# Optimization experiments

Hardware: AMD Instinct MI355X
Metric: run time of the kernel (lower is better)

## Reference

```python
import jax, jax.numpy as jnp
import numpy as np

B, S, D = 2, 2048, 1024
E, N, HID = 8, 4, 4096

def setup_inputs() -> dict:
    key = jax.random.key(0)
    ks = jax.random.split(key, 6)
    x = jax.random.normal(ks[0], (B, S, D), dtype=jnp.float32)
    w_router = jax.random.normal(ks[1], (E, D), dtype=jnp.float32) * 0.02
    A_fc = jax.random.normal(ks[2], (E, N, N, N), dtype=jnp.float32) * 0.5
    S_fc = jax.random.normal(ks[3], (E, N, HID // N, D // N), dtype=jnp.float32) * (1.0 / np.sqrt(D))
    A_proj = jax.random.normal(ks[4], (E, N, N, N), dtype=jnp.float32) * 0.5
    S_proj = jax.random.normal(ks[5], (E, N, D // N, HID // N), dtype=jnp.float32) * (1.0 / np.sqrt(HID))
    return {"x": x, "w_router": w_router, "A_fc": A_fc, "S_fc": S_fc, "A_proj": A_proj, "S_proj": S_proj}

def _phm(Xn, A, S):
    # Xn: [T, n, s_in], S: [n, s_out, s_in], A: [n, n, n] -> [T, n, s_out]
    T_ = jnp.einsum('bkl,iol->bkio', Xn, S)
    return jnp.einsum('ijk,bkio->bjo', A, T_)

def reference(x, w_router, A_fc, S_fc, A_proj, S_proj):
    e_num, n = A_fc.shape[0], A_fc.shape[1]
    d = x.shape[-1]
    flat = x.reshape(-1, d)                      # [T, D]
    T = flat.shape[0]
    logits = flat @ w_router.T                   # [T, E]
    probs = jax.nn.softmax(logits, axis=-1)
    expert_idx = jnp.argmax(logits, axis=-1)     # [T]
    tpe = jnp.zeros((e_num,), flat.dtype).at[expert_idx].add(1.0)
    frac = tpe / T
    aux_loss = jnp.sum(frac * probs.mean(axis=0)) * e_num
    Xn = flat.reshape(T, n, d // n)
    out = jnp.zeros_like(flat)
    for e in range(e_num):                        # small fixed expert loop
        h = _phm(Xn, A_fc[e], S_fc[e]).reshape(T, -1)   # [T, HID]
        h = jnp.where(h >= 0, h, 0.5 * h)               # leaky_relu slope 0.5
        Hn = (h * h).reshape(T, n, -1)
        y = _phm(Hn, A_proj[e], S_proj[e]).reshape(T, d)
        out = out + jnp.where((expert_idx == e)[:, None], y, jnp.zeros((), flat.dtype))
    return out.reshape(x.shape), aux_loss
```

## Files before the change

kernel.cpp:

```cpp
#include <hip/hip_runtime.h>
#include <hip/hip_bf16.h>


#define T_TOK 4096
#define DIM   1024
#define NEXP  8
#define HIDD  4096
#define SLOTS 5120

static constexpr size_t OFF_WFC   = 0;
static constexpr size_t OFF_WPROJ = 67108864ull;
static constexpr size_t OFF_XB    = 134217728ull;
static constexpr size_t OFF_H     = 144703488ull;
static constexpr size_t OFF_BSUM  = 186646528ull;
static constexpr size_t OFF_EIDX  = OFF_BSUM + 1024*8*8;
static constexpr size_t OFF_TOK   = OFF_EIDX + (size_t)T_TOK*4;
static constexpr size_t OFF_CNT   = OFF_TOK + (size_t)SLOTS*4;

typedef __attribute__((ext_vector_type(8))) short short8;
typedef __attribute__((ext_vector_type(4))) float f32x4;

static __device__ __forceinline__ ushort f2bf(float f) {
    __hip_bfloat16 h = __float2bfloat16(f);
    return __builtin_bit_cast(ushort, h);
}

static __device__ __forceinline__ ushort4 f4bf(float4 v) {
    ushort4 b;
    b.x = f2bf(v.x); b.y = f2bf(v.y); b.z = f2bf(v.z); b.w = f2bf(v.w);
    return b;
}

static __device__ __forceinline__ void gload_lds16(const ushort* g, ushort* l) {
    __builtin_amdgcn_global_load_lds((const __attribute__((address_space(1))) void*)g,
                                     (__attribute__((address_space(3))) void*)l,
                                     16, 0, 0);
}

__global__ __launch_bounds__(256) void front_k(const float* __restrict__ x,
                                               const float* __restrict__ wr,
                                               double* __restrict__ bsum,
                                               int* __restrict__ eidx,
                                               ushort* __restrict__ xb,
                                               const float* __restrict__ Afc,
                                               const float* __restrict__ Sfc,
                                               ushort* __restrict__ Wfc)
{
    __shared__ double shp[4][8];
    __shared__ float Ash[64];
    int tid = threadIdx.x;
    if (blockIdx.x < 1024) {
        int w = tid >> 6, lane = tid & 63;
        int t = blockIdx.x * 4 + w;
        const float4* xr = (const float4*)(x + (size_t)t * DIM);
        float4 xv[4];
#pragma unroll
        for (int q = 0; q < 4; q++) xv[q] = xr[q * 64 + lane];
        ushort4* xo = (ushort4*)(xb + (size_t)t * DIM);
#pragma unroll
        for (int q = 0; q < 4; q++) xo[q * 64 + lane] = f4bf(xv[q]);
        double lg[8];
#pragma unroll
        for (int e = 0; e < 8; e++) {
            const float4* wv = (const float4*)(wr + (size_t)e * DIM);
            double s = 0.0;
#pragma unroll
            for (int q = 0; q < 4; q++) {
                float4 a = xv[q], b = wv[q * 64 + lane];
                s += (double)a.x * b.x + (double)a.y * b.y + (double)a.z * b.z + (double)a.w * b.w;
            }
#pragma unroll
            for (int d = 1; d < 64; d <<= 1) s += __shfl_xor(s, d);
            lg[e] = s;
        }
        double m = lg[0];
#pragma unroll
        for (int e = 1; e < 8; e++) m = lg[e] > m ? lg[e] : m;
        double ex[8], sum = 0.0;
#pragma unroll
        for (int e = 0; e < 8; e++) { ex[e] = exp(lg[e] - m); sum += ex[e]; }
        if (lane < 8) shp[w][lane] = ex[lane] / sum;
        if (lane == 0) {
            int am = 0; double bv = lg[0];
#pragma unroll
            for (int e = 1; e < 8; e++) if (lg[e] > bv) { bv = lg[e]; am = e; }
            eidx[t] = am;
        }
        __syncthreads();
        if (tid < 8)
            bsum[(size_t)blockIdx.x * 8 + tid] =
                shp[0][tid] + shp[1][tid] + shp[2][tid] + shp[3][tid];
    } else {
        int b2 = blockIdx.x - 1024;
        int e = b2 >> 10, o = b2 & 1023;
        if (tid < 64) Ash[tid] = Afc[e * 64 + tid];
        __syncthreads();
        int k = tid >> 6, lq = tid & 63;
        float4 sv[4];
#pragma unroll
        for (int i = 0; i < 4; i++)
            sv[i] = *(const float4*)&Sfc[((size_t)(e * 4 + i) * 1024 + o) * 256 + lq * 4];
        size_t base = (size_t)e * 4194304ull;
#pragma unroll
        for (int j = 0; j < 4; j++) {
            float a0 = Ash[j * 4 + k], a1 = Ash[16 + j * 4 + k];
            float a2 = Ash[32 + j * 4 + k], a3 = Ash[48 + j * 4 + k];
            float4 v;
            v.x = a0 * sv[0].x + a1 * sv[1].x + a2 * sv[2].x + a3 * sv[3].x;
            v.y = a0 * sv[0].y + a1 * sv[1].y + a2 * sv[2].y + a3 * sv[3].y;
            v.z = a0 * sv[0].z + a1 * sv[1].z + a2 * sv[2].z + a3 * sv[3].z;
            v.w = a0 * sv[0].w + a1 * sv[1].w + a2 * sv[2].w + a3 * sv[3].w;
            *(ushort4*)&Wfc[base + (size_t)(j * 1024 + o) * 1024 + k * 256 + lq * 4] = f4bf(v);
        }
    }
}

__global__ __launch_bounds__(256) void plan_k(const double* __restrict__ bsum,
                                              const int* __restrict__ eidx,
                                              int* __restrict__ counts,
                                              int* __restrict__ offsets,
                                              int* __restrict__ tok,
                                              float* __restrict__ auxout)
{
    __shared__ int hist[256][8];
    __shared__ double red[256][8];
    __shared__ int offs[8];
    int tid = threadIdx.x;
    for (int i = tid; i < SLOTS; i += 256) tok[i] = -1;
    int base = tid * 16;
    int le[16];
    int lc[8] = {0,0,0,0,0,0,0,0};
#pragma unroll
    for (int j = 0; j < 16; j++) { le[j] = eidx[base + j]; lc[le[j]]++; }
#pragma unroll
    for (int e = 0; e < 8; e++) hist[tid][e] = lc[e];
    __syncthreads();
    for (int s = 1; s < 256; s <<= 1) {
        int v[8];
        if (tid >= s) {
#pragma unroll
            for (int e = 0; e < 8; e++) v[e] = hist[tid - s][e];
        }
        __syncthreads();
        if (tid >= s) {
#pragma unroll
            for (int e = 0; e < 8; e++) hist[tid][e] += v[e];
        }
        __syncthreads();
    }
    int myBase[8];
#pragma unroll
    for (int e = 0; e < 8; e++) myBase[e] = hist[tid][e] - lc[e];
    if (tid == 0) {
        int off = 0;
#pragma unroll
        for (int e = 0; e < 8; e++) {
            int c = hist[255][e];
            counts[e] = c;
            offsets[e] = off; offs[e] = off;
            off += (c + 127) & ~127;
        }
    }
    __syncthreads();
    int cur[8];
#pragma unroll
    for (int e = 0; e < 8; e++) cur[e] = myBase[e];
#pragma unroll
    for (int j = 0; j < 16; j++) {
        int e = le[j];
        tok[offs[e] + cur[e]++] = base + j;
    }
    double ps[8] = {0, 0, 0, 0, 0, 0, 0, 0};
    for (int b = tid; b < 1024; b += 256) {
#pragma unroll
        for (int e = 0; e < 8; e++) ps[e] += bsum[(size_t)b * 8 + e];
    }
#pragma unroll
    for (int e = 0; e < 8; e++) red[tid][e] = ps[e];
    __syncthreads();
    for (int s = 128; s > 0; s >>= 1) {
        if (tid < s) {
#pragma unroll
            for (int e = 0; e < 8; e++) red[tid][e] += red[tid + s][e];
        }
        __syncthreads();
    }
    if (tid == 0) {
        double aux = 0.0;
#pragma unroll
        for (int e = 0; e < 8; e++)
            aux += ((double)hist[255][e] / T_TOK) * (red[0][e] / T_TOK);
        auxout[0] = (float)(aux * NEXP);
    }
}

__global__ __launch_bounds__(256, 2) void mid_k(const ushort* __restrict__ xb,
                                                const ushort* __restrict__ Wfc,
                                                ushort* __restrict__ h,
                                                const int* __restrict__ counts,
                                                const int* __restrict__ offsets,
                                                const int* __restrict__ tok,
                                                const float* __restrict__ Apj,
                                                const float* __restrict__ Spj,
                                                ushort* __restrict__ Wpj)
{
    __shared__ __align__(16) ushort As[128 * 64];
    __shared__ __align__(16) ushort Bs[256 * 64];
    __shared__ float Ashf[64];
    int b = blockIdx.x;
    int tid = threadIdx.x;
    if (b >= 640) {
        int b2 = b - 640;
        int e = b2 >> 8, o = b2 & 255;
        if (tid < 64) Ashf[tid] = Apj[e * 64 + tid];
        __syncthreads();
        float4 sv[4];
#pragma unroll
        for (int i = 0; i < 4; i++)
            sv[i] = *(const float4*)&Spj[((size_t)(e * 4 + i) * 256 + o) * 1024 + tid * 4];
        size_t base = (size_t)e * 4194304ull;
#pragma unroll
        for (int j = 0; j < 4; j++)
#pragma unroll
            for (int k = 0; k < 4; k++) {
                float a0 = Ashf[j * 4 + k], a1 = Ashf[16 + j * 4 + k];
                float a2 = Ashf[32 + j * 4 + k], a3 = Ashf[48 + j * 4 + k];
                float4 v;
                v.x = a0 * sv[0].x + a1 * sv[1].x + a2 * sv[2].x + a3 * sv[3].x;
                v.y = a0 * sv[0].y + a1 * sv[1].y + a2 * sv[2].y + a3 * sv[3].y;
                v.z = a0 * sv[0].z + a1 * sv[1].z + a2 * sv[2].z + a3 * sv[3].z;
                v.w = a0 * sv[0].w + a1 * sv[1].w + a2 * sv[2].w + a3 * sv[3].w;
                *(ushort4*)&Wpj[base + (size_t)(j * 256 + o) * 4096 + k * 1024 + tid * 4] = f4bf(v);
            }
        return;
    }
    constexpr int KDIM = 1024;
    constexpr int NDIM = 4096;
    int r = b >> 3;
    int nb = (b & 7) * 2 + r / 40;
    int ms = r % 40;
    int e = -1, mt = 0, acct = 0;
#pragma unroll
    for (int i = 0; i < 8; i++) {
        int tiles = (counts[i] + 127) >> 7;
        if (e < 0 && ms < acct + tiles) { e = i; mt = ms - acct; }
        acct += tiles;
    }
    if (e < 0) return;
    int m_base = offsets[e] + mt * 128;
    int n_base = nb * 256;
    int w = tid >> 6, lane = tid & 63;
    int wm = w >> 1, wn = w & 1;
    const ushort* Bb = Wfc + (size_t)e * NDIM * KDIM + (size_t)n_base * KDIM;
    int lr = lane >> 3;
    int lcs = (((lane & 7) ^ lr) << 3);
    const ushort* arow[4];
#pragma unroll
    for (int i = 0; i < 4; i++) {
        int sl = m_base + i * 32 + w * 8 + lr;
        int rt = tok[sl]; if (rt < 0) rt = 0;
        arow[i] = xb + (size_t)rt * KDIM + lcs;
    }
    f32x4 acc[4][8];
#pragma unroll
    for (int i = 0; i < 4; i++)
#pragma unroll
        for (int j = 0; j < 8; j++) acc[i][j] = (f32x4){0.f, 0.f, 0.f, 0.f};

    for (int t = 0; t < KDIM / 64; t++) {
        int k0 = t * 64;
#pragma unroll
        for (int i = 0; i < 4; i++)
            gload_lds16(arow[i] + k0, &As[(i * 32 + w * 8) * 64]);
#pragma unroll
        for (int i = 0; i < 8; i++) {
            int r0 = i * 32 + w * 8;
            gload_lds16(Bb + (size_t)(r0 + lr) * KDIM + k0 + lcs, &Bs[r0 * 64]);
        }
        __syncthreads();
#pragma unroll
        for (int ks = 0; ks < 2; ks++) {
            short8 a[4], bfr[8];
            int ca = (((ks * 4 + (lane >> 4)) ^ (lane & 7)) << 3);
#pragma unroll
            for (int f = 0; f < 4; f++)
                a[f] = *(const short8*)&As[(wm * 64 + f * 16 + (lane & 15)) * 64 + ca];
#pragma unroll
            for (int f = 0; f < 8; f++)
                bfr[f] = *(const short8*)&Bs[(wn * 128 + f * 16 + (lane & 15)) * 64 + ca];
#pragma unroll
            for (int mf = 0; mf < 4; mf++)
#pragma unroll
                for (int nf = 0; nf < 8; nf++)
                    acc[mf][nf] = __builtin_amdgcn_mfma_f32_16x16x32_bf16(a[mf], bfr[nf], acc[mf][nf], 0, 0, 0);
        }
        __syncthreads();
    }

    int col0 = n_base + wn * 128;
    int row0 = wm * 64 + (lane >> 4) * 4;
#pragma unroll
    for (int mf = 0; mf < 4; mf++)
#pragma unroll
        for (int nf = 0; nf < 8; nf++) {
            int col = col0 + nf * 16 + (lane & 15);
#pragma unroll
            for (int rg = 0; rg < 4; rg++) {
                float v = acc[mf][nf][rg];
                v = v >= 0.f ? v : 0.5f * v;
                v = v * v;
                h[(size_t)(m_base + row0 + mf * 16 + rg) * NDIM + col] = f2bf(v);
            }
        }
}

__global__ __launch_bounds__(256, 2) void proj_k(const ushort* __restrict__ h,
                                                 const ushort* __restrict__ Wpj,
                                                 float* __restrict__ Part,
                                                 const int* __restrict__ counts,
                                                 const int* __restrict__ offsets)
{
    __shared__ __align__(16) ushort As[128 * 64];
    __shared__ __align__(16) ushort Bs[256 * 64];
    constexpr int KDIM = 4096;
    constexpr int NDIM = 1024;
    constexpr int KSUB = 2048;
    int b = blockIdx.x;
    int nb = (b & 7) >> 1;
    int split = b & 1;
    int ms = b >> 3;
    int e = -1, mt = 0, acct = 0;
#pragma unroll
    for (int i = 0; i < 8; i++) {
        int tiles = (counts[i] + 127) >> 7;
        if (e < 0 && ms < acct + tiles) { e = i; mt = ms - acct; }
        acct += tiles;
    }
    if (e < 0) return;
    int m_base = offsets[e] + mt * 128;
    int n_base = nb * 256;
    int tid = threadIdx.x, w = tid >> 6, lane = tid & 63;
    int wm = w >> 1, wn = w & 1;
    int lr = lane >> 3;
    int lcs = (((lane & 7) ^ lr) << 3);
    int kbase = split * KSUB;
    const ushort* Bb = Wpj + (size_t)e * NDIM * KDIM + (size_t)n_base * KDIM + kbase;
    const ushort* arow[4];
#pragma unroll
    for (int i = 0; i < 4; i++)
        arow[i] = h + (size_t)(m_base + i * 32 + w * 8 + lr) * KDIM + kbase + lcs;
    f32x4 acc[4][8];
#pragma unroll
    for (int i = 0; i < 4; i++)
#pragma unroll
        for (int j = 0; j < 8; j++) acc[i][j] = (f32x4){0.f, 0.f, 0.f, 0.f};

    for (int t = 0; t < KSUB / 64; t++) {
        int k0 = t * 64;
#pragma unroll
        for (int i = 0; i < 4; i++)
            gload_lds16(arow[i] + k0, &As[(i * 32 + w * 8) * 64]);
#pragma unroll
        for (int i = 0; i < 8; i++) {
            int r0 = i * 32 + w * 8;
            gload_lds16(Bb + (size_t)(r0 + lr) * KDIM + k0 + lcs, &Bs[r0 * 64]);
        }
        __syncthreads();
#pragma unroll
        for (int ks = 0; ks < 2; ks++) {
            short8 a[4], bfr[8];
            int ca = (((ks * 4 + (lane >> 4)) ^ (lane & 7)) << 3);
#pragma unroll
            for (int f = 0; f < 4; f++)
                a[f] = *(const short8*)&As[(wm * 64 + f * 16 + (lane & 15)) * 64 + ca];
#pragma unroll
            for (int f = 0; f < 8; f++)
                bfr[f] = *(const short8*)&Bs[(wn * 128 + f * 16 + (lane & 15)) * 64 + ca];
#pragma unroll
            for (int mf = 0; mf < 4; mf++)
#pragma unroll
                for (int nf = 0; nf < 8; nf++)
                    acc[mf][nf] = __builtin_amdgcn_mfma_f32_16x16x32_bf16(a[mf], bfr[nf], acc[mf][nf], 0, 0, 0);
        }
        __syncthreads();
    }

    float* P = Part + (size_t)split * SLOTS * NDIM;
    int col0 = n_base + wn * 128;
    int row0 = wm * 64 + (lane >> 4) * 4;
#pragma unroll
    for (int mf = 0; mf < 4; mf++)
#pragma unroll
        for (int nf = 0; nf < 8; nf++) {
            int col = col0 + nf * 16 + (lane & 15);
#pragma unroll
            for (int rg = 0; rg < 4; rg++)
                P[(size_t)(m_base + row0 + mf * 16 + rg) * NDIM + col] = acc[mf][nf][rg];
        }
}

__global__ __launch_bounds__(256) void reduce_k(const float* __restrict__ P,
                                                const int* __restrict__ tok,
                                                float* __restrict__ out)
{
    int slot = blockIdx.x;
    int t = tok[slot];
    if (t < 0) return;
    const float4* p0 = (const float4*)(P + (size_t)slot * DIM);
    const float4* p1 = (const float4*)(P + (size_t)(SLOTS + slot) * DIM);
    float4* o = (float4*)(out + (size_t)t * DIM);
    int i = threadIdx.x;
    float4 a = p0[i], b = p1[i];
    o[i] = (float4){a.x + b.x, a.y + b.y, a.z + b.z, a.w + b.w};
}

extern "C" void kernel_launch(void* const* d_in, const int* in_sizes, int n_in,
                              void* d_out, int out_size, void* d_ws, size_t ws_size,
                              hipStream_t stream)
{
    const float* x    = (const float*)d_in[0];
    const float* wr   = (const float*)d_in[1];
    const float* A_fc = (const float*)d_in[2];
    const float* S_fc = (const float*)d_in[3];
    const float* A_pj = (const float*)d_in[4];
    const float* S_pj = (const float*)d_in[5];
    float* out = (float*)d_out;
    char* ws = (char*)d_ws;

    ushort* Wfc   = (ushort*)(ws + OFF_WFC);
    float*  Part  = (float*)(ws + OFF_WFC);
    ushort* Wpj   = (ushort*)(ws + OFF_WPROJ);
    ushort* xb    = (ushort*)(ws + OFF_XB);
    ushort* h     = (ushort*)(ws + OFF_H);
    double* bsum  = (double*)(ws + OFF_BSUM);
    int*    eidx  = (int*)(ws + OFF_EIDX);
    int*    tok   = (int*)(ws + OFF_TOK);
    int*    counts  = (int*)(ws + OFF_CNT);
    int*    offsets = counts + 16;

    front_k<<<1024 + 8192, 256, 0, stream>>>(x, wr, bsum, eidx, xb, A_fc, S_fc, Wfc);
    plan_k<<<1, 256, 0, stream>>>(bsum, eidx, counts, offsets, tok,
                                  out + (size_t)T_TOK * DIM);
    mid_k<<<640 + 2048, 256, 0, stream>>>(xb, Wfc, h, counts, offsets, tok,
                                          A_pj, S_pj, Wpj);
    proj_k<<<320, 256, 0, stream>>>(h, Wpj, Part, counts, offsets);
    reduce_k<<<SLOTS, 256, 0, stream>>>(Part, tok, out);
}
```

Before: 175.4 us.

## Move fc weight build into plan kernel and store projection partials as bf16

The fc weight materialisation blocks move out of the router kernel and into the single-block plan kernel. The weight build now runs alongside the serial planning block instead of lengthening the front kernel. The split-K partial outputs of the projection GEMM are written as bf16 rather than fp32, halving partial write and reduce read traffic. This adds rounding error to the partial sums before the final fp32 add.

```diff
diff --git a/kernel.cpp b/kernel.cpp
--- a/kernel.cpp
+++ b/kernel.cpp
@@ -25,6 +25,10 @@
     return __builtin_bit_cast(ushort, h);
 }
 
+static __device__ __forceinline__ float bf2f(ushort u) {
+    return __builtin_bit_cast(float, (unsigned)u << 16);
+}
+
 static __device__ __forceinline__ ushort4 f4bf(float4 v) {
     ushort4 b;
     b.x = f2bf(v.x); b.y = f2bf(v.y); b.z = f2bf(v.z); b.w = f2bf(v.w);
@@ -41,57 +45,69 @@
                                                const float* __restrict__ wr,
                                                double* __restrict__ bsum,
                                                int* __restrict__ eidx,
-                                               ushort* __restrict__ xb,
-                                               const float* __restrict__ Afc,
-                                               const float* __restrict__ Sfc,
-                                               ushort* __restrict__ Wfc)
+                                               ushort* __restrict__ xb)
 {
     __shared__ double shp[4][8];
+    int tid = threadIdx.x;
+    int w = tid >> 6, lane = tid & 63;
+    int t = blockIdx.x * 4 + w;
+    const float4* xr = (const float4*)(x + (size_t)t * DIM);
+    float4 xv[4];
+#pragma unroll
+    for (int q = 0; q < 4; q++) xv[q] = xr[q * 64 + lane];
+    ushort4* xo = (ushort4*)(xb + (size_t)t * DIM);
+#pragma unroll
+    for (int q = 0; q < 4; q++) xo[q * 64 + lane] = f4bf(xv[q]);
+    double lg[8];
+#pragma unroll
+    for (int e = 0; e < 8; e++) {
+        const float4* wv = (const float4*)(wr + (size_t)e * DIM);
+        double s = 0.0;
+#pragma unroll
+        for (int q = 0; q < 4; q++) {
+            float4 a = xv[q], b = wv[q * 64 + lane];
+            s += (double)a.x * b.x + (double)a.y * b.y + (double)a.z * b.z + (double)a.w * b.w;
+        }
+#pragma unroll
+        for (int d = 1; d < 64; d <<= 1) s += __shfl_xor(s, d);
+        lg[e] = s;
+    }
+    double m = lg[0];
+#pragma unroll
+    for (int e = 1; e < 8; e++) m = lg[e] > m ? lg[e] : m;
+    double ex[8], sum = 0.0;
+#pragma unroll
+    for (int e = 0; e < 8; e++) { ex[e] = exp(lg[e] - m); sum += ex[e]; }
+    if (lane < 8) shp[w][lane] = ex[lane] / sum;
+    if (lane == 0) {
+        int am = 0; double bv = lg[0];
+#pragma unroll
+        for (int e = 1; e < 8; e++) if (lg[e] > bv) { bv = lg[e]; am = e; }
+        eidx[t] = am;
+    }
+    __syncthreads();
+    if (tid < 8)
+        bsum[(size_t)blockIdx.x * 8 + tid] =
+            shp[0][tid] + shp[1][tid] + shp[2][tid] + shp[3][tid];
+}
+
+__global__ __launch_bounds__(256) void plan_k(const double* __restrict__ bsum,
+                                              const int* __restrict__ eidx,
+                                              int* __restrict__ counts,
+                                              int* __restrict__ offsets,
+                                              int* __restrict__ tok,
+                                              float* __restrict__ auxout,
+                                              const float* __restrict__ Afc,
+                                              const float* __restrict__ Sfc,
+                                              ushort* __restrict__ Wfc)
+{
+    __shared__ int hist[256][8];
+    __shared__ double red[256][8];
+    __shared__ int offs[8];
     __shared__ float Ash[64];
     int tid = threadIdx.x;
-    if (blockIdx.x < 1024) {
-        int w = tid >> 6, lane = tid & 63;
-        int t = blockIdx.x * 4 + w;
-        const float4* xr = (const float4*)(x + (size_t)t * DIM);
-        float4 xv[4];
-#pragma unroll
-        for (int q = 0; q < 4; q++) xv[q] = xr[q * 64 + lane];
-        ushort4* xo = (ushort4*)(xb + (size_t)t * DIM);
-#pragma unroll
-        for (int q = 0; q < 4; q++) xo[q * 64 + lane] = f4bf(xv[q]);
-        double lg[8];
-#pragma unroll
-        for (int e = 0; e < 8; e++) {
-            const float4* wv = (const float4*)(wr + (size_t)e * DIM);
-            double s = 0.0;
-#pragma unroll
-            for (int q = 0; q < 4; q++) {
-                float4 a = xv[q], b = wv[q * 64 + lane];
-                s += (double)a.x * b.x + (double)a.y * b.y + (double)a.z * b.z + (double)a.w * b.w;
-            }
-#pragma unroll
-            for (int d = 1; d < 64; d <<= 1) s += __shfl_xor(s, d);
-            lg[e] = s;
-        }
-        double m = lg[0];
-#pragma unroll
-        for (int e = 1; e < 8; e++) m = lg[e] > m ? lg[e] : m;
-        double ex[8], sum = 0.0;
-#pragma unroll
-        for (int e = 0; e < 8; e++) { ex[e] = exp(lg[e] - m); sum += ex[e]; }
-        if (lane < 8) shp[w][lane] = ex[lane] / sum;
-        if (lane == 0) {
-            int am = 0; double bv = lg[0];
-#pragma unroll
-            for (int e = 1; e < 8; e++) if (lg[e] > bv) { bv = lg[e]; am = e; }
-            eidx[t] = am;
-        }
-        __syncthreads();
-        if (tid < 8)
-            bsum[(size_t)blockIdx.x * 8 + tid] =
-                shp[0][tid] + shp[1][tid] + shp[2][tid] + shp[3][tid];
-    } else {
-        int b2 = blockIdx.x - 1024;
+    if (blockIdx.x > 0) {
+        int b2 = blockIdx.x - 1;
         int e = b2 >> 10, o = b2 & 1023;
         if (tid < 64) Ash[tid] = Afc[e * 64 + tid];
         __syncthreads();
@@ -112,20 +128,8 @@
             v.w = a0 * sv[0].w + a1 * sv[1].w + a2 * sv[2].w + a3 * sv[3].w;
             *(ushort4*)&Wfc[base + (size_t)(j * 1024 + o) * 1024 + k * 256 + lq * 4] = f4bf(v);
         }
-    }
-}
-
-__global__ __launch_bounds__(256) void plan_k(const double* __restrict__ bsum,
-                                              const int* __restrict__ eidx,
-                                              int* __restrict__ counts,
-                                              int* __restrict__ offsets,
-                                              int* __restrict__ tok,
-                                              float* __restrict__ auxout)
-{
-    __shared__ int hist[256][8];
-    __shared__ double red[256][8];
-    __shared__ int offs[8];
-    int tid = threadIdx.x;
+        return;
+    }
     for (int i = tid; i < SLOTS; i += 256) tok[i] = -1;
     int base = tid * 16;
     int le[16];
@@ -316,7 +320,7 @@
 
 __global__ __launch_bounds__(256, 2) void proj_k(const ushort* __restrict__ h,
                                                  const ushort* __restrict__ Wpj,
-                                                 float* __restrict__ Part,
+                                                 ushort* __restrict__ Part,
                                                  const int* __restrict__ counts,
                                                  const int* __restrict__ offsets)
 {
@@ -385,7 +389,7 @@
         __syncthreads();
     }
 
-    float* P = Part + (size_t)split * SLOTS * NDIM;
+    ushort* P = Part + (size_t)split * SLOTS * NDIM;
     int col0 = n_base + wn * 128;
     int row0 = wm * 64 + (lane >> 4) * 4;
 #pragma unroll
@@ -395,23 +399,24 @@
             int col = col0 + nf * 16 + (lane & 15);
 #pragma unroll
             for (int rg = 0; rg < 4; rg++)
-                P[(size_t)(m_base + row0 + mf * 16 + rg) * NDIM + col] = acc[mf][nf][rg];
-        }
-}
-
-__global__ __launch_bounds__(256) void reduce_k(const float* __restrict__ P,
+                P[(size_t)(m_base + row0 + mf * 16 + rg) * NDIM + col] = f2bf(acc[mf][nf][rg]);
+        }
+}
+
+__global__ __launch_bounds__(256) void reduce_k(const ushort* __restrict__ P,
                                                 const int* __restrict__ tok,
                                                 float* __restrict__ out)
 {
     int slot = blockIdx.x;
     int t = tok[slot];
     if (t < 0) return;
-    const float4* p0 = (const float4*)(P + (size_t)slot * DIM);
-    const float4* p1 = (const float4*)(P + (size_t)(SLOTS + slot) * DIM);
+    int i = threadIdx.x;
+    const ushort4* p0 = (const ushort4*)(P + (size_t)slot * DIM);
+    const ushort4* p1 = (const ushort4*)(P + (size_t)(SLOTS + slot) * DIM);
+    ushort4 a = p0[i], b = p1[i];
     float4* o = (float4*)(out + (size_t)t * DIM);
-    int i = threadIdx.x;
-    float4 a = p0[i], b = p1[i];
-    o[i] = (float4){a.x + b.x, a.y + b.y, a.z + b.z, a.w + b.w};
+    o[i] = (float4){bf2f(a.x) + bf2f(b.x), bf2f(a.y) + bf2f(b.y),
+                    bf2f(a.z) + bf2f(b.z), bf2f(a.w) + bf2f(b.w)};
 }
 
 extern "C" void kernel_launch(void* const* d_in, const int* in_sizes, int n_in,
@@ -428,7 +433,7 @@
     char* ws = (char*)d_ws;
 
     ushort* Wfc   = (ushort*)(ws + OFF_WFC);
-    float*  Part  = (float*)(ws + OFF_WFC);
+    ushort* Part  = (ushort*)(ws + OFF_WFC);
     ushort* Wpj   = (ushort*)(ws + OFF_WPROJ);
     ushort* xb    = (ushort*)(ws + OFF_XB);
     ushort* h     = (ushort*)(ws + OFF_H);
@@ -438,9 +443,10 @@
     int*    counts  = (int*)(ws + OFF_CNT);
     int*    offsets = counts + 16;
 
-    front_k<<<1024 + 8192, 256, 0, stream>>>(x, wr, bsum, eidx, xb, A_fc, S_fc, Wfc);
-    plan_k<<<1, 256, 0, stream>>>(bsum, eidx, counts, offsets, tok,
-                                  out + (size_t)T_TOK * DIM);
+    front_k<<<T_TOK / 4, 256, 0, stream>>>(x, wr, bsum, eidx, xb);
+    plan_k<<<1 + 8192, 256, 0, stream>>>(bsum, eidx, counts, offsets, tok,
+                                         out + (size_t)T_TOK * DIM,
+                                         A_fc, S_fc, Wfc);
     mid_k<<<640 + 2048, 256, 0, stream>>>(xb, Wfc, h, counts, offsets, tok,
                                           A_pj, S_pj, Wpj);
     proj_k<<<320, 256, 0, stream>>>(h, Wpj, Part, counts, offsets);
```

Measured after the change: 167.5 us (median of 2 runs). 4.5% less time.
